# Kernel optimization log

Measured on AMD Instinct MI355X. Metric: run time of the kernel, lower is better.

The kernel has to match this reference:

```python
import jax, jax.numpy as jnp
import numpy as np

# Powderworld element-id mapping (channel 0 holds the element id as a float)
ELEM = {'empty': 0, 'sand': 1, 'water': 3, 'wall': 2, 'plant': 5, 'stone': 6,
        'lava': 8, 'gas': 9, 'wood': 7, 'ice': 10, 'fire': 11, 'dust': 13,
        'acid': 12, 'cloner': 4, 'agentKangaroo': 14, 'agentLemming': 15}
NUM_ELEMS = 16
B, C, H, W = 16, 20, 512, 512


def _get_bool(world, name):
    return world[:, 0:1] == ELEM[name]


def _roll_left(x):
    return jnp.roll(x, shift=1, axis=3)


def _roll_right(x):
    return jnp.roll(x, shift=-1, axis=3)


def setup_inputs() -> dict:
    key = jax.random.key(0)
    k1, k2, k3, k4, k5, k6, k7 = jax.random.split(key, 7)
    world = jax.random.normal(k1, (B, C, H, W), dtype=jnp.float32) * 0.1
    # channel 0: element ids; channel 2: gravity flag in {0,1}; channel 8: did-gravity flag
    ids = jax.random.randint(k2, (B, 1, H, W), 0, NUM_ELEMS).astype(jnp.float32)
    grav = jax.random.bernoulli(k3, 0.8, (B, 1, H, W)).astype(jnp.float32)
    didg = jax.random.bernoulli(k4, 0.2, (B, 1, H, W)).astype(jnp.float32)
    world = world.at[:, 0:1].set(ids).at[:, 2:3].set(grav).at[:, 8:9].set(didg)
    rand_movement = jax.random.uniform(k5, (B, 1, H, W), dtype=jnp.float32)
    rand_interact = jax.random.uniform(k6, (B, 1, H, W), dtype=jnp.float32)
    rand_element = jax.random.uniform(k7, (B, 1, H, W), dtype=jnp.float32)
    return {'world': world, 'rand_movement': rand_movement,
            'rand_interact': rand_interact, 'rand_element': rand_element}


def reference(world, rand_movement, rand_interact, rand_element):
    f32 = world.dtype
    new_fluid_momentum = jnp.zeros_like(world[:, 0:1])
    for fall_left in (True, False):
        get_in_dir = _roll_left if fall_left else _roll_right
        get_in_not_dir = _roll_right if fall_left else _roll_left
        fall_dir = (rand_movement + world[:, 6:7] + new_fluid_momentum) > 0.5
        is_matching_fall = fall_dir if fall_left else ~fall_dir
        world_left = get_in_dir(world)
        world_right = get_in_not_dir(world)
        is_air_move = _get_bool(world, 'agentKangaroo') | _get_bool(world, 'agentLemming')
        is_element = (_get_bool(world, 'empty') | _get_bool(world, 'water')
                      | _get_bool(world, 'gas') | _get_bool(world, 'lava')
                      | _get_bool(world, 'acid') | is_air_move)
        is_left_density_lower = (world[:, 1:2] - world_left[:, 1:2]) > 0
        is_gravity = world[:, 2:3] == 1
        is_left_gravity = world_left[:, 2:3] == 1
        not_did_gravity_left = (~(world[:, 8:9] > 0)) | is_air_move
        does_become_left = (is_matching_fall & is_element & not_did_gravity_left
                            & is_left_density_lower & is_left_gravity & is_gravity)
        does_become_right = get_in_not_dir(does_become_left)
        has_overlap = does_become_left & does_become_right
        does_become_left_real = does_become_left & ~has_overlap
        does_become_right_real = get_in_not_dir(does_become_left_real)
        new_fluid_momentum = new_fluid_momentum + does_become_right_real.astype(f32) * (2.0 if fall_left else -2.0)
        # interp2: (~a & ~b)*world + a*world_left + b*world_right
        a = does_become_left_real.astype(f32)
        b = does_become_right_real.astype(f32)
        neither = (~does_become_left_real & ~does_become_right_real).astype(f32)
        world = neither * world + a * world_left + b * world_right
    is_fluid = (_get_bool(world, 'empty') | _get_bool(world, 'water')
                | _get_bool(world, 'gas') | _get_bool(world, 'lava')
                | _get_bool(world, 'acid') | _get_bool(world, 'agentKangaroo')
                | _get_bool(world, 'agentLemming'))
    mom = jnp.where(is_fluid, new_fluid_momentum, world[:, 6:7])
    world = world.at[:, 6:7].set(mom)
    return world
```

## Files before the change

### kernel.cpp

```cpp
#include <hip/hip_runtime.h>


#define WW 512
#define HH 512
#define CC 20
#define BB 16

__device__ __forceinline__ bool is_fluid_id(float id) {
    return (id == 0.0f) | (id == 3.0f) | (id == 9.0f) | (id == 8.0f) |
           (id == 12.0f) | (id == 14.0f) | (id == 15.0f);
}

__global__ __launch_bounds__(512)
void fluid_flow_kernel(const float* __restrict__ world,
                       const float* __restrict__ rand_movement,
                       float* __restrict__ out) {
    __shared__ __attribute__((aligned(16))) float id_s[WW];
    __shared__ __attribute__((aligned(16))) float den_s[WW];
    __shared__ __attribute__((aligned(16))) float grav_s[WW];
    __shared__ __attribute__((aligned(16))) float mom_s[WW];
    __shared__ __attribute__((aligned(16))) float didg_s[WW];
    __shared__ __attribute__((aligned(16))) float rm_s[WW];
    __shared__ __attribute__((aligned(16))) float momout_s[WW];
    __shared__ int   dbl_s[WW];
    __shared__ int   s1_s[WW];
    __shared__ short sfin_s[WW];
    __shared__ __attribute__((aligned(16))) float buf[2][4][WW];

    const int row = blockIdx.x;
    const int b   = row >> 9;
    const int h   = row & (HH - 1);
    const int x   = threadIdx.x;

    const size_t plane   = (size_t)HH * WW;
    const size_t baseRow = ((size_t)b * CC * HH + (size_t)h) * WW;
    const size_t rrow    = ((size_t)b * HH + (size_t)h) * WW;

    {
        int f = x;
        #pragma unroll
        for (int it = 0; it < 2; ++it, f += 512) {
            if (f < 768) {
                const int a  = f >> 7;
                const int q4 = f & 127;
                const float4* sp;
                float* dp;
                switch (a) {
                    case 0: sp = (const float4*)(world + baseRow);             dp = id_s;   break;
                    case 1: sp = (const float4*)(world + baseRow + plane);     dp = den_s;  break;
                    case 2: sp = (const float4*)(world + baseRow + 2 * plane); dp = grav_s; break;
                    case 3: sp = (const float4*)(world + baseRow + 6 * plane); dp = mom_s;  break;
                    case 4: sp = (const float4*)(world + baseRow + 8 * plane); dp = didg_s; break;
                    default: sp = (const float4*)(rand_movement + rrow);       dp = rm_s;   break;
                }
                ((float4*)dp)[q4] = sp[q4];
            }
        }
    }
    __syncthreads();

    {
        const float fd  = rm_s[x] + mom_s[x];
        const bool matching = fd > 0.5f;
        const float idc = id_s[x];
        const bool ia = (idc == 14.0f) | (idc == 15.0f);
        const bool ie = (idc == 0.0f) | (idc == 3.0f) | (idc == 9.0f) |
                        (idc == 8.0f) | (idc == 12.0f) | ia;
        const int  xl  = (x - 1) & (WW - 1);
        const bool ldl = (den_s[x] - den_s[xl]) > 0.0f;
        const bool ig  = grav_s[x]  == 1.0f;
        const bool ilg = grav_s[xl] == 1.0f;
        const bool ndg = (!(didg_s[x] > 0.0f)) | ia;
        dbl_s[x] = (matching & ie & ndg & ldl & ilg & ig) ? 1 : 0;
    }
    __syncthreads();

    float nfm;
    {
        const int d0 = dbl_s[x];
        const int d1 = dbl_s[(x + 1) & (WW - 1)];
        const int d2 = dbl_s[(x + 2) & (WW - 1)];
        const bool a1 = d0 && !d1;
        const bool b1 = d1 && !d2;
        s1_s[x] = a1 ? ((x - 1) & (WW - 1)) : (b1 ? ((x + 1) & (WW - 1)) : x);
        nfm = b1 ? 2.0f : 0.0f;
    }
    __syncthreads();

    {
        const int c = s1_s[x];
        const int l = s1_s[(x + 1) & (WW - 1)];
        const float fd = (rm_s[x] + mom_s[c]) + nfm;
        const bool matching = !(fd > 0.5f);
        const float idc = id_s[c];
        const bool ia = (idc == 14.0f) | (idc == 15.0f);
        const bool ie = (idc == 0.0f) | (idc == 3.0f) | (idc == 9.0f) |
                        (idc == 8.0f) | (idc == 12.0f) | ia;
        const bool ldl = (den_s[c] - den_s[l]) > 0.0f;
        const bool ig  = grav_s[c] == 1.0f;
        const bool ilg = grav_s[l] == 1.0f;
        const bool ndg = (!(didg_s[c] > 0.0f)) | ia;
        const bool d = matching & ie & ndg & ldl & ilg & ig;
        __syncthreads();
        dbl_s[x] = d ? 1 : 0;
    }
    __syncthreads();

    {
        const int d0  = dbl_s[x];
        const int dm1 = dbl_s[(x - 1) & (WW - 1)];
        const int dm2 = dbl_s[(x - 2) & (WW - 1)];
        const bool a2 = d0  && !dm1;
        const bool b2 = dm1 && !dm2;
        const int s2  = a2 ? ((x + 1) & (WW - 1)) : (b2 ? ((x - 1) & (WW - 1)) : x);
        const int sx  = s1_s[s2];
        const float nfm_final = nfm + (b2 ? -2.0f : 0.0f);
        const bool fluid = is_fluid_id(id_s[sx]);
        momout_s[x] = fluid ? nfm_final : mom_s[sx];
        sfin_s[x]   = (short)sx;
    }
    __syncthreads();

    const int slot = x >> 7;
    const int q    = x & 127;

    #pragma unroll
    for (int g = 0; g < 5; ++g) {
        const int c = 4 * g + slot;
        float* bslot = buf[g & 1][slot];

        float4 v;
        if      (c == 0) v = ((const float4*)id_s)[q];
        else if (c == 1) v = ((const float4*)den_s)[q];
        else if (c == 2) v = ((const float4*)grav_s)[q];
        else if (c == 6) v = ((const float4*)momout_s)[q];
        else if (c == 8) v = ((const float4*)didg_s)[q];
        else             v = *(const float4*)(world + baseRow + (size_t)c * plane + 4 * q);
        ((float4*)bslot)[q] = v;
        __syncthreads();

        float* op = out + baseRow + (size_t)c * plane;
        #pragma unroll
        for (int j = 0; j < 4; ++j) {
            const int m   = q + 128 * j;
            const int src = (c == 6) ? m : (int)sfin_s[m];
            op[m] = bslot[src];
        }
    }
}

extern "C" void kernel_launch(void* const* d_in, const int* in_sizes, int n_in,
                              void* d_out, int out_size, void* d_ws, size_t ws_size,
                              hipStream_t stream) {
    const float* world = (const float*)d_in[0];
    const float* rm    = (const float*)d_in[1];
    float* out = (float*)d_out;

    dim3 grid(BB * HH);
    dim3 block(WW);
    fluid_flow_kernel<<<grid, block, 0, stream>>>(world, rm, out);
}
```

Baseline: 554.9 us.

## Load all channels to LDS via direct global-to-LDS loads, vectorize gathered output stores

Each row's channels, including the 15 previously streamed ones, are now loaded up front into shared memory with global_load_lds 16-byte transfers spread across wavefronts. The per-channel double-buffered loop with a barrier per iteration is removed, and the output is written as float4 stores gathered through the final source indices held in registers. This is meant to issue all global reads early, remove barriers and widen the stores. In exchange, shared memory per block grows to about 50 KB, which may reduce occupancy.

```diff
diff --git a/kernel.cpp b/kernel.cpp
--- a/kernel.cpp
+++ b/kernel.cpp
@@ -1,10 +1,17 @@
 #include <hip/hip_runtime.h>
+#include <stdint.h>
 
 
 #define WW 512
 #define HH 512
 #define CC 20
 #define BB 16
+
+__device__ __forceinline__ void gload_lds16(const float* g, float* l) {
+    __builtin_amdgcn_global_load_lds((__attribute__((address_space(1))) void*)(g),
+                                     (__attribute__((address_space(3))) void*)(l),
+                                     16, 0, 0);
+}
 
 __device__ __forceinline__ bool is_fluid_id(float id) {
     return (id == 0.0f) | (id == 3.0f) | (id == 9.0f) | (id == 8.0f) |
@@ -22,41 +29,47 @@
     __shared__ __attribute__((aligned(16))) float didg_s[WW];
     __shared__ __attribute__((aligned(16))) float rm_s[WW];
     __shared__ __attribute__((aligned(16))) float momout_s[WW];
+    __shared__ __attribute__((aligned(16))) float chbuf[15][WW];
     __shared__ int   dbl_s[WW];
     __shared__ int   s1_s[WW];
-    __shared__ short sfin_s[WW];
-    __shared__ __attribute__((aligned(16))) float buf[2][4][WW];
+    __shared__ __attribute__((aligned(16))) short sfin_s[WW];
 
-    const int row = blockIdx.x;
-    const int b   = row >> 9;
-    const int h   = row & (HH - 1);
-    const int x   = threadIdx.x;
+    const int row  = blockIdx.x;
+    const int b    = row >> 9;
+    const int h    = row & (HH - 1);
+    const int x    = threadIdx.x;
+    const int lane = x & 63;
+    const int wv   = x >> 6;
 
     const size_t plane   = (size_t)HH * WW;
     const size_t baseRow = ((size_t)b * CC * HH + (size_t)h) * WW;
     const size_t rrow    = ((size_t)b * HH + (size_t)h) * WW;
 
-    {
-        int f = x;
-        #pragma unroll
-        for (int it = 0; it < 2; ++it, f += 512) {
-            if (f < 768) {
-                const int a  = f >> 7;
-                const int q4 = f & 127;
-                const float4* sp;
-                float* dp;
-                switch (a) {
-                    case 0: sp = (const float4*)(world + baseRow);             dp = id_s;   break;
-                    case 1: sp = (const float4*)(world + baseRow + plane);     dp = den_s;  break;
-                    case 2: sp = (const float4*)(world + baseRow + 2 * plane); dp = grav_s; break;
-                    case 3: sp = (const float4*)(world + baseRow + 6 * plane); dp = mom_s;  break;
-                    case 4: sp = (const float4*)(world + baseRow + 8 * plane); dp = didg_s; break;
-                    default: sp = (const float4*)(rand_movement + rrow);       dp = rm_s;   break;
-                }
-                ((float4*)dp)[q4] = sp[q4];
+    for (int k = wv; k < 42; k += 8) {
+        const float* gsrc;
+        float*       ldst;
+        if (k < 12) {
+            const int a   = k >> 1;
+            const int off = (k & 1) * 256;
+            switch (a) {
+                case 0:  gsrc = world + baseRow + off;             ldst = id_s   + off; break;
+                case 1:  gsrc = world + baseRow + plane + off;     ldst = den_s  + off; break;
+                case 2:  gsrc = world + baseRow + 2 * plane + off; ldst = grav_s + off; break;
+                case 3:  gsrc = world + baseRow + 6 * plane + off; ldst = mom_s  + off; break;
+                case 4:  gsrc = world + baseRow + 8 * plane + off; ldst = didg_s + off; break;
+                default: gsrc = rand_movement + rrow + off;        ldst = rm_s   + off; break;
             }
+        } else {
+            const int kk   = k - 12;
+            const int ci   = kk >> 1;
+            const int off  = (kk & 1) * 256;
+            const int ach  = ci + 3 + (ci >= 3) + (ci >= 4);
+            gsrc = world + baseRow + (size_t)ach * plane + off;
+            ldst = &chbuf[ci][off];
         }
+        gload_lds16(gsrc + lane * 4, ldst);
     }
+    asm volatile("s_waitcnt vmcnt(0)" ::: "memory");
     __syncthreads();
 
     {
@@ -100,9 +113,7 @@
         const bool ig  = grav_s[c] == 1.0f;
         const bool ilg = grav_s[l] == 1.0f;
         const bool ndg = (!(didg_s[c] > 0.0f)) | ia;
-        const bool d = matching & ie & ndg & ldl & ilg & ig;
-        __syncthreads();
-        dbl_s[x] = d ? 1 : 0;
+        dbl_s[x] = (matching & ie & ndg & ldl & ilg & ig) ? 1 : 0;
     }
     __syncthreads();
 
@@ -123,29 +134,25 @@
 
     const int slot = x >> 7;
     const int q    = x & 127;
+    const short4 s4 = ((const short4*)sfin_s)[q];
+    const int i0 = s4.x, i1 = s4.y, i2 = s4.z, i3 = s4.w;
 
     #pragma unroll
-    for (int g = 0; g < 5; ++g) {
-        const int c = 4 * g + slot;
-        float* bslot = buf[g & 1][slot];
-
+    for (int i = 0; i < 5; ++i) {
+        const int c = slot + 4 * i;
         float4 v;
-        if      (c == 0) v = ((const float4*)id_s)[q];
-        else if (c == 1) v = ((const float4*)den_s)[q];
-        else if (c == 2) v = ((const float4*)grav_s)[q];
-        else if (c == 6) v = ((const float4*)momout_s)[q];
-        else if (c == 8) v = ((const float4*)didg_s)[q];
-        else             v = *(const float4*)(world + baseRow + (size_t)c * plane + 4 * q);
-        ((float4*)bslot)[q] = v;
-        __syncthreads();
-
-        float* op = out + baseRow + (size_t)c * plane;
-        #pragma unroll
-        for (int j = 0; j < 4; ++j) {
-            const int m   = q + 128 * j;
-            const int src = (c == 6) ? m : (int)sfin_s[m];
-            op[m] = bslot[src];
+        if (c == 6) {
+            v = ((const float4*)momout_s)[q];
+        } else {
+            const float* src;
+            if      (c == 0) src = id_s;
+            else if (c == 1) src = den_s;
+            else if (c == 2) src = grav_s;
+            else if (c == 8) src = didg_s;
+            else             src = chbuf[c - 3 - (c > 6) - (c > 8)];
+            v.x = src[i0]; v.y = src[i1]; v.z = src[i2]; v.w = src[i3];
         }
+        *(float4*)(out + baseRow + (size_t)c * plane + 4 * q) = v;
     }
 }
 
```

After: 558.2 us. Within noise of the previous version (+0.6%).
